# Kernel optimization log

Hardware: AMD Instinct MI355X
Metric: run time of the kernel (lower is better)

## Reference

```python
import jax, jax.numpy as jnp
import numpy as np

N0 = N1 = 100000
D = H = 512
E = 1000000
NEG_SLOPE = 0.01  # nn.LeakyReLU default

def _lin(k, fin, fout):
    kw, kb = jax.random.split(k)
    s = 1.0 / np.sqrt(fin)
    W = jax.random.uniform(kw, (fin, fout), jnp.float32, -s, s)
    b = jax.random.uniform(kb, (fout,), jnp.float32, -s, s)
    return W, b

def setup_inputs() -> dict:
    key = jax.random.key(0)
    ks = jax.random.split(key, 18)
    inp = {
        "x_n0": jax.random.normal(ks[0], (N0, D), jnp.float32),
        "x_n1": jax.random.normal(ks[1], (N1, D), jnp.float32),
        "ei_01": jnp.stack([jax.random.randint(ks[2], (E,), 0, N0),
                            jax.random.randint(ks[3], (E,), 0, N1)]),
        "ei_10": jnp.stack([jax.random.randint(ks[4], (E,), 0, N1),
                            jax.random.randint(ks[5], (E,), 0, N0)]),
    }
    i = 6
    for layer, din in (("l1", D), ("l2", H)):
        for mt in ("01", "10"):
            Wn, bn = _lin(ks[i], din, H); i += 1
            Ws, bs = _lin(ks[i], din, H); i += 1
            Wu, bu = _lin(ks[i], 2 * H, H); i += 1
            inp[f"{layer}_{mt}_Wn"] = Wn; inp[f"{layer}_{mt}_bn"] = bn
            inp[f"{layer}_{mt}_Ws"] = Ws; inp[f"{layer}_{mt}_bs"] = bs
            inp[f"{layer}_{mt}_Wu"] = Wu; inp[f"{layer}_{mt}_bu"] = bu
    return inp

def _sage(x_src, x_dst, ei, Wn, bn, Ws, bs, Wu, bu):
    # HeteroSAGEConv: gather src feats along edges, mean-aggregate onto dst,
    # then lin_neigh(agg) || lin_self(x_dst) -> lin_update
    n_dst = x_dst.shape[0]
    agg = jax.ops.segment_sum(x_src[ei[0]], ei[1], num_segments=n_dst)  # [n_dst, d]
    cnt = jax.ops.segment_sum(jnp.ones((ei.shape[1],), x_src.dtype), ei[1], num_segments=n_dst)
    agg = agg / jnp.maximum(cnt, 1.0)[:, None]
    h = jnp.concatenate([agg @ Wn + bn, x_dst @ Ws + bs], axis=-1)  # [n_dst, 2H]
    return h @ Wu + bu

def _lrelu(x):
    return jax.nn.leaky_relu(x, NEG_SLOPE)

def reference(x_n0, x_n1, ei_01, ei_10,
              l1_01_Wn, l1_01_bn, l1_01_Ws, l1_01_bs, l1_01_Wu, l1_01_bu,
              l1_10_Wn, l1_10_bn, l1_10_Ws, l1_10_bs, l1_10_Wu, l1_10_bu,
              l2_01_Wn, l2_01_bn, l2_01_Ws, l2_01_bs, l2_01_Wu, l2_01_bu,
              l2_10_Wn, l2_10_bn, l2_10_Ws, l2_10_bs, l2_10_Wu, l2_10_bu):
    # dropout is identity in eval mode (p handled outside the math)
    h0, h1 = _lrelu(x_n0), _lrelu(x_n1)
    o1 = _sage(h0, h1, ei_01, l1_01_Wn, l1_01_bn, l1_01_Ws, l1_01_bs, l1_01_Wu, l1_01_bu)
    o0 = _sage(h1, h0, ei_10, l1_10_Wn, l1_10_bn, l1_10_Ws, l1_10_bs, l1_10_Wu, l1_10_bu)
    h0, h1 = _lrelu(o0), _lrelu(o1)
    o1 = _sage(h0, h1, ei_01, l2_01_Wn, l2_01_bn, l2_01_Ws, l2_01_bs, l2_01_Wu, l2_01_bu)
    o0 = _sage(h1, h0, ei_10, l2_10_Wn, l2_10_bn, l2_10_Ws, l2_10_bs, l2_10_Wu, l2_10_bu)
    return (o0, o1)
```

## Files before the change

kernel.cpp:

```cpp
#include <hip/hip_runtime.h>


typedef unsigned short ushort_t;
using short8 = __attribute__((ext_vector_type(8))) short;
using f32x4  = __attribute__((ext_vector_type(4))) float;

typedef __attribute__((address_space(3))) void lds_void;
typedef __attribute__((address_space(1))) void gbl_void;

__device__ __forceinline__ void gload16(const void* g, void* l) {
  __builtin_amdgcn_global_load_lds((gbl_void*)g, (lds_void*)l, 16, 0, 0);
}

__device__ __forceinline__ float bf2f(unsigned short u) {
  union { unsigned i; float f; } c; c.i = ((unsigned)u) << 16; return c.f;
}
__device__ __forceinline__ unsigned short f2bf(float f) {
  union { float f; unsigned i; } c; c.f = f;
  unsigned r = c.i + 0x7FFF + ((c.i >> 16) & 1);
  return (unsigned short)(r >> 16);
}
__device__ __forceinline__ unsigned pack2(float a, float b) {
  return (unsigned)f2bf(a) | ((unsigned)f2bf(b) << 16);
}

template <int MODE>
__device__ __forceinline__ void gemm_core(
    const ushort_t* __restrict__ A0, const ushort_t* __restrict__ A1,
    int lda, int ka0,
    const ushort_t* __restrict__ BT, int ldb,
    const float* __restrict__ bias,
    void* __restrict__ outp, int ldo, int Mreal, int Ktiles,
    int bm, int bn)
{
  __shared__ __align__(16) ushort_t lA[128 * 32];
  __shared__ __align__(16) ushort_t lB[128 * 32];
  const int tid = threadIdx.x;
  const int w = tid >> 6;
  const int l = tid & 63;
  const int srow = (l >> 2);
  const int scol = (l & 3) * 8;
  const int m_base = bm * 128;
  const int n_base = bn * 128;

  f32x4 acc[4][4] = {};

  for (int kt = 0; kt < Ktiles; ++kt) {
    const int k0 = kt * 32;
    const ushort_t* As; int kk;
    if (k0 < ka0) { As = A0; kk = k0; } else { As = A1; kk = k0 - ka0; }
#pragma unroll
    for (int r = 0; r < 2; ++r) {
      const int row = r * 64 + w * 16 + srow;
      gload16(As + (size_t)(m_base + row) * lda + (kk + scol),
              lA + (size_t)(r * 64 + w * 16) * 32);
      gload16(BT + (size_t)(n_base + row) * ldb + (k0 + scol),
              lB + (size_t)(r * 64 + w * 16) * 32);
    }
    __syncthreads();

    const int wm0 = (w & 1) * 64;
    const int wn0 = (w >> 1) * 64;
    const int fr  = l & 15;
    const int fko = (l >> 4) * 8;
    short8 a[4], b[4];
#pragma unroll
    for (int t = 0; t < 4; ++t) {
      a[t] = *(const short8*)&lA[(wm0 + t * 16 + fr) * 32 + fko];
      b[t] = *(const short8*)&lB[(wn0 + t * 16 + fr) * 32 + fko];
    }
#pragma unroll
    for (int mt = 0; mt < 4; ++mt)
#pragma unroll
      for (int nt = 0; nt < 4; ++nt)
        acc[mt][nt] = __builtin_amdgcn_mfma_f32_16x16x32_bf16(
            a[mt], b[nt], acc[mt][nt], 0, 0, 0);
    __syncthreads();
  }

  const int wm0 = (w & 1) * 64;
  const int wn0 = (w >> 1) * 64;
  const int quad = l >> 4;
  const int c15 = l & 15;
#pragma unroll
  for (int nt = 0; nt < 4; ++nt) {
    const int gn = n_base + wn0 + nt * 16 + c15;
    const float bv = (MODE == 2) ? 0.0f : bias[gn];
#pragma unroll
    for (int mt = 0; mt < 4; ++mt) {
#pragma unroll
      for (int r = 0; r < 4; ++r) {
        const int gm = m_base + wm0 + mt * 16 + quad * 4 + r;
        float v = acc[mt][nt][r] + bv;
        if (MODE == 0) {
          if (gm < Mreal) ((float*)outp)[(size_t)gm * ldo + gn] = v;
        } else if (MODE == 1) {
          float t = v > 0.0f ? v : 0.01f * v;
          ((ushort_t*)outp)[(size_t)gm * ldo + gn] = f2bf(t);
        } else {
          ((ushort_t*)outp)[(size_t)gn * ldo + gm] = f2bf(v);
        }
      }
    }
  }
}

struct GemmArgs {
  const ushort_t* A0; const ushort_t* A1; int lda; int ka0;
  const ushort_t* BT; int ldb; const float* bias;
  void* out; int ldo; int Mreal; int Ktiles;
};

template <int MODE>
__global__ __launch_bounds__(256) void gemm_kernel(GemmArgs g) {
  gemm_core<MODE>(g.A0, g.A1, g.lda, g.ka0, g.BT, g.ldb, g.bias,
                  g.out, g.ldo, g.Mreal, g.Ktiles, blockIdx.x, blockIdx.y);
}

__global__ __launch_bounds__(256) void fold_gemm_kernel(
    const ushort_t* __restrict__ WnWs, const ushort_t* __restrict__ WuT,
    ushort_t* __restrict__ WfT)
{
  const int z = blockIdx.z, sage = z >> 1, half = z & 1;
  gemm_core<2>(WnWs + (size_t)sage * 524288 + half * 262144, nullptr, 512, (1 << 30),
               WuT + (size_t)sage * 524288 + half * 512, 1024, nullptr,
               WfT + (size_t)sage * 524288 + half * 512, 1024, 512, 16,
               blockIdx.x, blockIdx.y);
}

__global__ void lrelu_cast_kernel(const float* __restrict__ x,
                                  ushort_t* __restrict__ h, int n4)
{
  const int i = blockIdx.x * 256 + threadIdx.x;
  if (i >= n4) return;
  const float4 v = ((const float4*)x)[i];
  float a = v.x > 0.f ? v.x : 0.01f * v.x;
  float b = v.y > 0.f ? v.y : 0.01f * v.y;
  float c = v.z > 0.f ? v.z : 0.01f * v.z;
  float d = v.w > 0.f ? v.w : 0.01f * v.w;
  uint2 o; o.x = pack2(a, b); o.y = pack2(c, d);
  ((uint2*)h)[i] = o;
}

struct EdgeArgs {
  const int* src0; const int* dst0;
  const int* src1; const int* dst1;
  int* cnt0; int* cnt1;
  int* indptr0; int* indptr1;
  int* fill0; int* fill1;
  int* esrc0; int* esrc1;
  int E; int nd0; int nd1;
};

__global__ void hist_kernel(EdgeArgs ea) {
  const int dir = blockIdx.y;
  const int e = blockIdx.x * 256 + threadIdx.x;
  if (e >= ea.E) return;
  const int* dst = dir ? ea.dst1 : ea.dst0;
  int* cnt = dir ? ea.cnt1 : ea.cnt0;
  atomicAdd(&cnt[dst[e]], 1);
}

__global__ __launch_bounds__(1024) void scan_kernel(EdgeArgs ea) {
  const int dir = blockIdx.y;
  const int* cnt = dir ? ea.cnt1 : ea.cnt0;
  int* indptr = dir ? ea.indptr1 : ea.indptr0;
  int* fill = dir ? ea.fill1 : ea.fill0;
  const int n = dir ? ea.nd1 : ea.nd0;
  __shared__ int sd[1024];
  const int t = threadIdx.x;
  const int chunk = (n + 1023) >> 10;
  const int start = t * chunk;
  const int end = (start + chunk < n) ? (start + chunk) : n;
  int sum = 0;
  for (int i = start; i < end; ++i) sum += cnt[i];
  sd[t] = sum;
  __syncthreads();
  for (int off = 1; off < 1024; off <<= 1) {
    int v = (t >= off) ? sd[t - off] : 0;
    __syncthreads();
    sd[t] += v;
    __syncthreads();
  }
  int run = sd[t] - sum;
  for (int i = start; i < end; ++i) { indptr[i] = run; fill[i] = run; run += cnt[i]; }
  if (t == 0) indptr[n] = ea.E;
}

__global__ void scatter_kernel(EdgeArgs ea) {
  const int dir = blockIdx.y;
  const int e = blockIdx.x * 256 + threadIdx.x;
  if (e >= ea.E) return;
  const int* dst = dir ? ea.dst1 : ea.dst0;
  const int* src = dir ? ea.src1 : ea.src0;
  int* fill = dir ? ea.fill1 : ea.fill0;
  int* esrc = dir ? ea.esrc1 : ea.esrc0;
  const int pos = atomicAdd(&fill[dst[e]], 1);
  esrc[pos] = src[e];
}

__device__ __forceinline__ void acc8(float* a, uint4 u) {
  a[0] += bf2f((unsigned short)(u.x & 0xffff)); a[1] += bf2f((unsigned short)(u.x >> 16));
  a[2] += bf2f((unsigned short)(u.y & 0xffff)); a[3] += bf2f((unsigned short)(u.y >> 16));
  a[4] += bf2f((unsigned short)(u.z & 0xffff)); a[5] += bf2f((unsigned short)(u.z >> 16));
  a[6] += bf2f((unsigned short)(u.w & 0xffff)); a[7] += bf2f((unsigned short)(u.w >> 16));
}

__global__ __launch_bounds__(256) void agg_kernel(
    const ushort_t* __restrict__ hsrc, const int* __restrict__ indptr,
    const int* __restrict__ esrc, ushort_t* __restrict__ out, int ndst)
{
  const int widx = blockIdx.x * 4 + (threadIdx.x >> 6);
  const int l = threadIdx.x & 63;
  if (widx >= ndst) return;
  const int s = indptr[widx], e = indptr[widx + 1];
  float a[8] = {0.f, 0.f, 0.f, 0.f, 0.f, 0.f, 0.f, 0.f};
  int i = s;
  for (; i + 1 < e; i += 2) {
    const int r0 = esrc[i], r1 = esrc[i + 1];
    const uint4 u0 = *(const uint4*)(hsrc + (size_t)r0 * 512 + l * 8);
    const uint4 u1 = *(const uint4*)(hsrc + (size_t)r1 * 512 + l * 8);
    acc8(a, u0); acc8(a, u1);
  }
  if (i < e) {
    const uint4 u = *(const uint4*)(hsrc + (size_t)esrc[i] * 512 + l * 8);
    acc8(a, u);
  }
  const int deg = e - s;
  const float sc = 1.0f / (float)(deg > 1 ? deg : 1);
  uint4 o;
  o.x = pack2(a[0] * sc, a[1] * sc); o.y = pack2(a[2] * sc, a[3] * sc);
  o.z = pack2(a[4] * sc, a[5] * sc); o.w = pack2(a[6] * sc, a[7] * sc);
  *(uint4*)(out + (size_t)widx * 512 + l * 8) = o;
}

struct CastArgs { const float* Wn[4]; const float* Ws[4]; const float* Wu[4]; };

__global__ void cast_all_kernel(CastArgs ca, ushort_t* __restrict__ WnWs,
                                ushort_t* __restrict__ WuT)
{
  const int sage = blockIdx.z;
  const int type = blockIdx.y;
  const int idx = blockIdx.x * 256 + threadIdx.x;
  if (type < 2) {
    if (idx >= 512 * 512) return;
    const float* src = type == 0 ? ca.Wn[sage] : ca.Ws[sage];
    WnWs[(size_t)sage * 524288 + type * 262144 + idx] = f2bf(src[idx]);
  } else {
    if (idx >= 1024 * 512) return;
    const int k = idx >> 9, n = idx & 511;
    WuT[(size_t)sage * 524288 + (size_t)n * 1024 + k] = f2bf(ca.Wu[sage][idx]);
  }
}

struct BiasArgs { const float* bn[4]; const float* bs[4];
                  const float* Wu[4]; const float* bu[4]; };

__global__ void bias_fold_kernel(BiasArgs ba, float* __restrict__ cf) {
  const int sage = blockIdx.y;
  const int n = blockIdx.x * 256 + threadIdx.x;
  const float* Wu = ba.Wu[sage];
  const float* bn = ba.bn[sage];
  const float* bs = ba.bs[sage];
  float s = ba.bu[sage][n];
  for (int j = 0; j < 512; ++j)
    s += bn[j] * Wu[(size_t)j * 512 + n] + bs[j] * Wu[(size_t)(512 + j) * 512 + n];
  cf[sage * 512 + n] = s;
}

extern "C" void kernel_launch(void* const* d_in, const int* in_sizes, int n_in,
                              void* d_out, int out_size, void* d_ws, size_t ws_size,
                              hipStream_t stream)
{
  const int Dm = 512;
  const int N0 = in_sizes[0] / Dm;
  const int N1 = in_sizes[1] / Dm;
  const int E  = in_sizes[2] / 2;
  const int NMAX = N0 > N1 ? N0 : N1;
  const int MP = ((NMAX + 127) / 128) * 128;
  const int Mtiles = MP / 128;

  auto al = [](size_t x) { return (x + 255) & ~(size_t)255; };
  const size_t BIG = (size_t)MP * 512 * sizeof(ushort_t);

  char* p = (char*)d_ws;
  ushort_t* h0 = (ushort_t*)p; p += BIG;
  ushort_t* h1 = (ushort_t*)p; p += BIG;
  ushort_t* bA = (ushort_t*)p; p += BIG;
  ushort_t* bB = (ushort_t*)p; p += BIG;
  ushort_t* bC = (ushort_t*)p; p += BIG;
  ushort_t* WnWs = (ushort_t*)p; p += al((size_t)4 * 524288 * 2);
  ushort_t* WuT  = (ushort_t*)p; p += al((size_t)4 * 524288 * 2);
  ushort_t* WfT  = (ushort_t*)p; p += al((size_t)4 * 524288 * 2);
  float* cf = (float*)p; p += al(4 * 512 * sizeof(float));
  char* cnt_base = p;
  int* cnt0 = (int*)p; p += al((size_t)N1 * 4);
  int* cnt1 = (int*)p; p += al((size_t)N0 * 4);
  const size_t cnt_bytes = (size_t)(p - cnt_base);
  int* ip0 = (int*)p; p += al((size_t)(N1 + 1) * 4);
  int* ip1 = (int*)p; p += al((size_t)(N0 + 1) * 4);
  int* fl0 = (int*)p; p += al((size_t)N1 * 4);
  int* fl1 = (int*)p; p += al((size_t)N0 * 4);
  int* es0 = (int*)p; p += al((size_t)E * 4);
  int* es1 = (int*)p; p += al((size_t)E * 4);
  if ((size_t)(p - (char*)d_ws) > ws_size) return;

  const float* x0 = (const float*)d_in[0];
  const float* x1 = (const float*)d_in[1];
  const int* ei01 = (const int*)d_in[2];
  const int* ei10 = (const int*)d_in[3];

  CastArgs ca; BiasArgs ba;
  for (int s = 0; s < 4; ++s) {
    const int base = 4 + 6 * s;
    ca.Wn[s] = (const float*)d_in[base + 0];
    ba.bn[s] = (const float*)d_in[base + 1];
    ca.Ws[s] = (const float*)d_in[base + 2];
    ba.bs[s] = (const float*)d_in[base + 3];
    ca.Wu[s] = (const float*)d_in[base + 4];
    ba.Wu[s] = ca.Wu[s];
    ba.bu[s] = (const float*)d_in[base + 5];
  }

  EdgeArgs ea;
  ea.src0 = ei01; ea.dst0 = ei01 + E;
  ea.src1 = ei10; ea.dst1 = ei10 + E;
  ea.cnt0 = cnt0; ea.cnt1 = cnt1;
  ea.indptr0 = ip0; ea.indptr1 = ip1;
  ea.fill0 = fl0; ea.fill1 = fl1;
  ea.esrc0 = es0; ea.esrc1 = es1;
  ea.E = E; ea.nd0 = N1; ea.nd1 = N0;

  hipMemsetAsync(cnt_base, 0, cnt_bytes, stream);
  lrelu_cast_kernel<<<dim3((N0 * Dm / 4 + 255) / 256), 256, 0, stream>>>(x0, h0, N0 * Dm / 4);
  lrelu_cast_kernel<<<dim3((N1 * Dm / 4 + 255) / 256), 256, 0, stream>>>(x1, h1, N1 * Dm / 4);
  hist_kernel<<<dim3((E + 255) / 256, 2), 256, 0, stream>>>(ea);
  scan_kernel<<<dim3(1, 2), 1024, 0, stream>>>(ea);
  scatter_kernel<<<dim3((E + 255) / 256, 2), 256, 0, stream>>>(ea);

  cast_all_kernel<<<dim3(2048, 3, 4), 256, 0, stream>>>(ca, WnWs, WuT);
  fold_gemm_kernel<<<dim3(4, 4, 8), 256, 0, stream>>>(WnWs, WuT, WfT);
  bias_fold_kernel<<<dim3(2, 4), 256, 0, stream>>>(ba, cf);

  agg_kernel<<<dim3((N1 + 3) / 4), 256, 0, stream>>>(h0, ip0, es0, bA, N1);
  agg_kernel<<<dim3((N0 + 3) / 4), 256, 0, stream>>>(h1, ip1, es1, bB, N0);

  GemmArgs g;
  g.lda = 512; g.ka0 = 512; g.ldb = 1024; g.Ktiles = 32; g.ldo = 512;
  g.A0 = bA; g.A1 = h1; g.BT = WfT + 0 * 524288; g.bias = cf + 0;
  g.out = bC; g.Mreal = N1;
  gemm_kernel<1><<<dim3(Mtiles, 4), 256, 0, stream>>>(g);
  g.A0 = bB; g.A1 = h0; g.BT = WfT + 1 * 524288; g.bias = cf + 512;
  g.out = bA; g.Mreal = N0;
  gemm_kernel<1><<<dim3(Mtiles, 4), 256, 0, stream>>>(g);

  agg_kernel<<<dim3((N1 + 3) / 4), 256, 0, stream>>>(bA, ip0, es0, h0, N1);
  agg_kernel<<<dim3((N0 + 3) / 4), 256, 0, stream>>>(bC, ip1, es1, h1, N0);

  g.A0 = h0; g.A1 = bC; g.BT = WfT + 2 * 524288; g.bias = cf + 1024;
  g.out = (float*)d_out + (size_t)N0 * 512; g.Mreal = N1;
  gemm_kernel<0><<<dim3(Mtiles, 4), 256, 0, stream>>>(g);
  g.A0 = h1; g.A1 = bA; g.BT = WfT + 3 * 524288; g.bias = cf + 1536;
  g.out = (float*)d_out; g.Mreal = N0;
  gemm_kernel<0><<<dim3(Mtiles, 4), 256, 0, stream>>>(g);
}
```

Before: 2.655 ms.

## Double-buffer GEMM LDS tiles and swizzle workgroups across XCDs

The GEMM core now uses two LDS buffers per operand. The next K-tile's global-to-LDS load is issued before computing on the current tile, so load latency overlaps MFMA work and one barrier per iteration is removed. The 2D grid becomes a 1D grid whose block index is remapped so consecutive tiles (sharing A rows across the 4 N tiles) land on the same XCD, improving L2 reuse. The cost is double the LDS use, which may lower occupancy, and the loop now assumes Ktiles is even.

Measured after the change: 2.647 ms. Within noise of the previous version (-0.3%).

```diff
diff --git a/kernel.cpp b/kernel.cpp
--- a/kernel.cpp
+++ b/kernel.cpp
@@ -33,8 +33,8 @@
     void* __restrict__ outp, int ldo, int Mreal, int Ktiles,
     int bm, int bn)
 {
-  __shared__ __align__(16) ushort_t lA[128 * 32];
-  __shared__ __align__(16) ushort_t lB[128 * 32];
+  __shared__ __align__(16) ushort_t lA[2][128 * 32];
+  __shared__ __align__(16) ushort_t lB[2][128 * 32];
   const int tid = threadIdx.x;
   const int w = tid >> 6;
   const int l = tid & 63;
@@ -45,7 +45,7 @@
 
   f32x4 acc[4][4] = {};
 
-  for (int kt = 0; kt < Ktiles; ++kt) {
+  auto stage = [&](int buf, int kt) {
     const int k0 = kt * 32;
     const ushort_t* As; int kk;
     if (k0 < ka0) { As = A0; kk = k0; } else { As = A1; kk = k0 - ka0; }
@@ -53,21 +53,23 @@
     for (int r = 0; r < 2; ++r) {
       const int row = r * 64 + w * 16 + srow;
       gload16(As + (size_t)(m_base + row) * lda + (kk + scol),
-              lA + (size_t)(r * 64 + w * 16) * 32);
+              &lA[buf][(r * 64 + w * 16) * 32]);
       gload16(BT + (size_t)(n_base + row) * ldb + (k0 + scol),
-              lB + (size_t)(r * 64 + w * 16) * 32);
+              &lB[buf][(r * 64 + w * 16) * 32]);
     }
-    __syncthreads();
-
-    const int wm0 = (w & 1) * 64;
-    const int wn0 = (w >> 1) * 64;
-    const int fr  = l & 15;
-    const int fko = (l >> 4) * 8;
+  };
+
+  const int wm0 = (w & 1) * 64;
+  const int wn0 = (w >> 1) * 64;
+  const int fr  = l & 15;
+  const int fko = (l >> 4) * 8;
+
+  auto compute = [&](int buf) {
     short8 a[4], b[4];
 #pragma unroll
     for (int t = 0; t < 4; ++t) {
-      a[t] = *(const short8*)&lA[(wm0 + t * 16 + fr) * 32 + fko];
-      b[t] = *(const short8*)&lB[(wn0 + t * 16 + fr) * 32 + fko];
+      a[t] = *(const short8*)&lA[buf][(wm0 + t * 16 + fr) * 32 + fko];
+      b[t] = *(const short8*)&lB[buf][(wn0 + t * 16 + fr) * 32 + fko];
     }
 #pragma unroll
     for (int mt = 0; mt < 4; ++mt)
@@ -75,11 +77,20 @@
       for (int nt = 0; nt < 4; ++nt)
         acc[mt][nt] = __builtin_amdgcn_mfma_f32_16x16x32_bf16(
             a[mt], b[nt], acc[mt][nt], 0, 0, 0);
+  };
+
+  stage(0, 0);
+  __syncthreads();
+
+  for (int kt = 0; kt < Ktiles; kt += 2) {
+    stage(1, kt + 1);
+    compute(0);
     __syncthreads();
-  }
-
-  const int wm0 = (w & 1) * 64;
-  const int wn0 = (w >> 1) * 64;
+    if (kt + 2 < Ktiles) stage(0, kt + 2);
+    compute(1);
+    __syncthreads();
+  }
+
   const int quad = l >> 4;
   const int c15 = l & 15;
 #pragma unroll
@@ -113,8 +124,14 @@
 
 template <int MODE>
 __global__ __launch_bounds__(256) void gemm_kernel(GemmArgs g) {
+  const int nwg = gridDim.x;
+  const int orig = blockIdx.x;
+  const int q = nwg >> 3, r = nwg & 7, x = orig & 7;
+  const int swz = (x < r ? x * (q + 1) : r * (q + 1) + (x - r) * q) + (orig >> 3);
+  const int bn = swz & 3;
+  const int bm = swz >> 2;
   gemm_core<MODE>(g.A0, g.A1, g.lda, g.ka0, g.BT, g.ldb, g.bias,
-                  g.out, g.ldo, g.Mreal, g.Ktiles, blockIdx.x, blockIdx.y);
+                  g.out, g.ldo, g.Mreal, g.Ktiles, bm, bn);
 }
 
 __global__ __launch_bounds__(256) void fold_gemm_kernel(
@@ -347,20 +364,21 @@
 
   GemmArgs g;
   g.lda = 512; g.ka0 = 512; g.ldb = 1024; g.Ktiles = 32; g.ldo = 512;
+  const int NWG = Mtiles * 4;
   g.A0 = bA; g.A1 = h1; g.BT = WfT + 0 * 524288; g.bias = cf + 0;
   g.out = bC; g.Mreal = N1;
-  gemm_kernel<1><<<dim3(Mtiles, 4), 256, 0, stream>>>(g);
+  gemm_kernel<1><<<dim3(NWG), 256, 0, stream>>>(g);
   g.A0 = bB; g.A1 = h0; g.BT = WfT + 1 * 524288; g.bias = cf + 512;
   g.out = bA; g.Mreal = N0;
-  gemm_kernel<1><<<dim3(Mtiles, 4), 256, 0, stream>>>(g);
+  gemm_kernel<1><<<dim3(NWG), 256, 0, stream>>>(g);
 
   agg_kernel<<<dim3((N1 + 3) / 4), 256, 0, stream>>>(bA, ip0, es0, h0, N1);
   agg_kernel<<<dim3((N0 + 3) / 4), 256, 0, stream>>>(bC, ip1, es1, h1, N0);
 
   g.A0 = h0; g.A1 = bC; g.BT = WfT + 2 * 524288; g.bias = cf + 1024;
   g.out = (float*)d_out + (size_t)N0 * 512; g.Mreal = N1;
-  gemm_kernel<0><<<dim3(Mtiles, 4), 256, 0, stream>>>(g);
+  gemm_kernel<0><<<dim3(NWG), 256, 0, stream>>>(g);
   g.A0 = h1; g.A1 = bA; g.BT = WfT + 3 * 524288; g.bias = cf + 1536;
   g.out = (float*)d_out; g.Mreal = N0;
-  gemm_kernel<0><<<dim3(Mtiles, 4), 256, 0, stream>>>(g);
-}
+  gemm_kernel<0><<<dim3(NWG), 256, 0, stream>>>(g);
+}
```
